# Kernel tuning notes

Measured on AMD Instinct MI355X. Metric: run time of the kernel, lower is better.

## Reference

```python
import jax, jax.numpy as jnp
import numpy as np

N_NODES = 20000
EPS_BN = 1e-5
NEG_SLOPE = 0.2


def gat_conv(x, W, att_src, att_dst, bias, src, dst, heads, out_ch, concat):
    n = x.shape[0]
    h = (x @ W).reshape(n, heads, out_ch)                       # [N,H,C]
    a_src = jnp.sum(h * att_src, axis=-1)                       # [N,H]
    a_dst = jnp.sum(h * att_dst, axis=-1)                       # [N,H]
    e = jax.nn.leaky_relu(a_src[src] + a_dst[dst], NEG_SLOPE)   # [E,H]
    # segment softmax over incoming edges of each destination node
    m = jax.ops.segment_max(e, dst, num_segments=n)             # [N,H]
    e = jnp.exp(e - m[dst])
    denom = jax.ops.segment_sum(e, dst, num_segments=n)         # [N,H]
    alpha = e / (denom[dst] + 1e-16)                            # [E,H]
    msg = alpha[:, :, None] * h[src]                            # [E,H,C]
    out = jax.ops.segment_sum(msg, dst, num_segments=n)         # [N,H,C]
    if concat:
        out = out.reshape(n, heads * out_ch)
    else:
        out = out.mean(axis=1)
    return out + bias


def batch_norm(x, gamma, beta):
    mu = x.mean(axis=0)
    var = x.var(axis=0)  # biased, matches torch normalization
    return (x - mu) * jax.lax.rsqrt(var + EPS_BN) * gamma + beta


def setup_inputs() -> dict:
    key = jax.random.key(0)
    ks = jax.random.split(key, 16)
    n, d_in, hid, heads = N_NODES, 768, 128, 8
    n_edges = 160000
    x = jax.random.normal(ks[0], (n, d_in), dtype=jnp.float32)
    edge_index = jax.random.randint(ks[1], (2, n_edges), 0, n, dtype=jnp.int64)
    s = lambda fi, fo: (2.0 / (fi + fo)) ** 0.5
    return {
        "x": x,
        "edge_index": edge_index,
        "W1": jax.random.normal(ks[2], (d_in, heads * hid), jnp.float32) * s(d_in, heads * hid),
        "att_src1": jax.random.normal(ks[3], (heads, hid), jnp.float32) * 0.1,
        "att_dst1": jax.random.normal(ks[4], (heads, hid), jnp.float32) * 0.1,
        "bias1": jnp.zeros((heads * hid,), jnp.float32),
        "bn1_g": jnp.ones((heads * hid,), jnp.float32),
        "bn1_b": jnp.zeros((heads * hid,), jnp.float32),
        "W2": jax.random.normal(ks[5], (heads * hid, hid), jnp.float32) * s(heads * hid, hid),
        "att_src2": jax.random.normal(ks[6], (1, hid), jnp.float32) * 0.1,
        "att_dst2": jax.random.normal(ks[7], (1, hid), jnp.float32) * 0.1,
        "bias2": jnp.zeros((hid,), jnp.float32),
        "bn2_g": jnp.ones((hid,), jnp.float32),
        "bn2_b": jnp.zeros((hid,), jnp.float32),
        "Wc1": jax.random.normal(ks[8], (hid, 64), jnp.float32) * s(hid, 64),
        "bc1": jnp.zeros((64,), jnp.float32),
        "Wc2": jax.random.normal(ks[9], (64, 2), jnp.float32) * s(64, 2),
        "bc2": jnp.zeros((2,), jnp.float32),
    }


def reference(x, edge_index, W1, att_src1, att_dst1, bias1, bn1_g, bn1_b,
              W2, att_src2, att_dst2, bias2, bn2_g, bn2_b,
              Wc1, bc1, Wc2, bc2):
    n = x.shape[0]
    # PyG GATConv default: add self-loops
    loops = jnp.arange(n, dtype=edge_index.dtype)
    src = jnp.concatenate([edge_index[0], loops])
    dst = jnp.concatenate([edge_index[1], loops])

    h = gat_conv(x, W1, att_src1, att_dst1, bias1, src, dst, heads=8, out_ch=128, concat=True)
    h = jax.nn.elu(batch_norm(h, bn1_g, bn1_b))
    # dropout disabled (deterministic reference)
    h = gat_conv(h, W2, att_src2, att_dst2, bias2, src, dst, heads=1, out_ch=128, concat=False)
    h = jax.nn.elu(batch_norm(h, bn2_g, bn2_b))
    h = jax.nn.elu(h @ Wc1 + bc1)
    return h @ Wc2 + bc2  # [N, 2] logits
```

## Files before the change

kernel.cpp:

```cpp
#include <hip/hip_runtime.h>
#include <stdint.h>

typedef unsigned short u16;
typedef __bf16 bf16x8 __attribute__((ext_vector_type(8)));
typedef float f32x4 __attribute__((ext_vector_type(4)));

__device__ __forceinline__ float b2f(u16 u) {
    unsigned x = ((unsigned)u) << 16;
    return __builtin_bit_cast(float, x);
}
__device__ __forceinline__ u16 f2b(float f) {
    unsigned x = __builtin_bit_cast(unsigned, f);
    x = x + 0x7fffu + ((x >> 16) & 1u);
    return (u16)(x >> 16);
}
__device__ __forceinline__ float leaky(float v) { return v > 0.f ? v : 0.2f * v; }
__device__ __forceinline__ float elu(float v) { return v > 0.f ? v : expm1f(v); }

__global__ void k_cast4(const float* __restrict__ in, u16* __restrict__ out, size_t n4) {
    size_t i = blockIdx.x * (size_t)blockDim.x + threadIdx.x;
    size_t stride = (size_t)gridDim.x * blockDim.x;
    for (; i < n4; i += stride) {
        float4 v = ((const float4*)in)[i];
        ushort4 o;
        o.x = f2b(v.x); o.y = f2b(v.y); o.z = f2b(v.z); o.w = f2b(v.w);
        ((ushort4*)out)[i] = o;
    }
}

__global__ void k_tcast(const float* __restrict__ in, u16* __restrict__ out, int R, int C) {
    __shared__ float tile[32][33];
    int tx = threadIdx.x & 31, ty = threadIdx.x >> 5;
    int c0 = blockIdx.x * 32, r0 = blockIdx.y * 32;
    #pragma unroll
    for (int i = 0; i < 32; i += 8) {
        int r = r0 + ty + i, c = c0 + tx;
        tile[ty + i][tx] = (r < R && c < C) ? in[(size_t)r * C + c] : 0.f;
    }
    __syncthreads();
    #pragma unroll
    for (int i = 0; i < 32; i += 8) {
        int c = c0 + ty + i, r = r0 + tx;
        if (c < C && r < R) out[(size_t)c * R + r] = f2b(tile[tx][ty + i]);
    }
}

#define GBM 128
#define GBN 128
#define GBK 64
#define LDT 72
#define SPLITK 4

__global__ __launch_bounds__(256) void k_gemm(const u16* __restrict__ A, const u16* __restrict__ Bt,
                                              u16* __restrict__ C, int M, int NN, int K, int nCB) {
    __shared__ __align__(16) u16 As[GBM][LDT];
    __shared__ __align__(16) u16 Bs[GBN][LDT];
    int nwg = gridDim.x, orig = blockIdx.x;
    int q = nwg >> 3, r8 = nwg & 7, xcd = orig & 7, sub = orig >> 3;
    int wgid = (xcd < r8 ? xcd * (q + 1) : r8 * (q + 1) + (xcd - r8) * q) + sub;
    int rb = wgid / nCB, cb = wgid % nCB;
    int brow = rb * GBM, bcol = cb * GBN;

    int t = threadIdx.x;
    int lane = t & 63, wid = t >> 6;
    int wm = (wid >> 1) * 64, wn = (wid & 1) * 64;
    int fr = lane & 15, fq = lane >> 4;
    f32x4 acc[4][4] = {};
    int tr = t >> 3, tc = (t & 7) * 8;
    int nK = K / GBK;
    for (int kt = 0; kt < nK; ++kt) {
        int k0 = kt * GBK;
        #pragma unroll
        for (int rr = 0; rr < 4; ++rr) {
            int r = tr + rr * 32;
            int grow = brow + r;
            uint4 bv = *reinterpret_cast<const uint4*>(Bt + (size_t)(bcol + r) * K + k0 + tc);
            *reinterpret_cast<uint4*>(&Bs[r][tc]) = bv;
            uint4 av = make_uint4(0, 0, 0, 0);
            if (grow < M) av = *reinterpret_cast<const uint4*>(A + (size_t)grow * K + k0 + tc);
            *reinterpret_cast<uint4*>(&As[r][tc]) = av;
        }
        __syncthreads();
        #pragma unroll
        for (int kk = 0; kk < 2; ++kk) {
            int ko = kk * 32 + fq * 8;
            bf16x8 af[4], bg[4];
            #pragma unroll
            for (int i = 0; i < 4; ++i) {
                af[i] = *reinterpret_cast<const bf16x8*>(&As[wm + i * 16 + fr][ko]);
                bg[i] = *reinterpret_cast<const bf16x8*>(&Bs[wn + i * 16 + fr][ko]);
            }
            #pragma unroll
            for (int mi = 0; mi < 4; ++mi)
                #pragma unroll
                for (int ni = 0; ni < 4; ++ni)
                    acc[mi][ni] = __builtin_amdgcn_mfma_f32_16x16x32_bf16(af[mi], bg[ni], acc[mi][ni], 0, 0, 0);
        }
        __syncthreads();
    }
    #pragma unroll
    for (int mi = 0; mi < 4; ++mi) {
        #pragma unroll
        for (int j = 0; j < 4; ++j) {
            int row = brow + wm + mi * 16 + fq * 4 + j;
            if (row < M) {
                #pragma unroll
                for (int ni = 0; ni < 4; ++ni) {
                    int col = bcol + wn + ni * 16 + fr;
                    C[(size_t)row * NN + col] = f2b(acc[mi][ni][j]);
                }
            }
        }
    }
}

__global__ __launch_bounds__(256) void k_gemm2(const u16* __restrict__ A, const u16* __restrict__ Bt,
                                               float* __restrict__ Cp, int M, int K,
                                               const float* __restrict__ scA, const float* __restrict__ shA) {
    __shared__ __align__(16) u16 As[GBM][LDT];
    __shared__ __align__(16) u16 Bs[GBN][LDT];
    int brow = blockIdx.x * GBM;
    int ks = blockIdx.y;
    int kBase = ks * (K / SPLITK);
    int t = threadIdx.x;
    int lane = t & 63, wid = t >> 6;
    int wm = (wid >> 1) * 64, wn = (wid & 1) * 64;
    int fr = lane & 15, fq = lane >> 4;
    f32x4 acc[4][4] = {};
    int tr = t >> 3, tc = (t & 7) * 8;
    const int nK = 1024 / SPLITK / GBK;
    for (int kt = 0; kt < nK; ++kt) {
        int k0 = kBase + kt * GBK;
        #pragma unroll
        for (int rr = 0; rr < 4; ++rr) {
            int r = tr + rr * 32;
            int grow = brow + r;
            uint4 bv = *reinterpret_cast<const uint4*>(Bt + (size_t)r * K + k0 + tc);
            *reinterpret_cast<uint4*>(&Bs[r][tc]) = bv;
            uint4 av = make_uint4(0, 0, 0, 0);
            if (grow < M) {
                uint4 u = *reinterpret_cast<const uint4*>(A + (size_t)grow * K + k0 + tc);
                float4 s0 = *(const float4*)(scA + k0 + tc);
                float4 s1 = *(const float4*)(scA + k0 + tc + 4);
                float4 h0 = *(const float4*)(shA + k0 + tc);
                float4 h1 = *(const float4*)(shA + k0 + tc + 4);
                u16 w0 = f2b(elu(b2f((u16)(u.x & 0xffff)) * s0.x + h0.x));
                u16 w1 = f2b(elu(b2f((u16)(u.x >> 16))    * s0.y + h0.y));
                u16 w2 = f2b(elu(b2f((u16)(u.y & 0xffff)) * s0.z + h0.z));
                u16 w3 = f2b(elu(b2f((u16)(u.y >> 16))    * s0.w + h0.w));
                u16 w4 = f2b(elu(b2f((u16)(u.z & 0xffff)) * s1.x + h1.x));
                u16 w5 = f2b(elu(b2f((u16)(u.z >> 16))    * s1.y + h1.y));
                u16 w6 = f2b(elu(b2f((u16)(u.w & 0xffff)) * s1.z + h1.z));
                u16 w7 = f2b(elu(b2f((u16)(u.w >> 16))    * s1.w + h1.w));
                av.x = (unsigned)w0 | ((unsigned)w1 << 16);
                av.y = (unsigned)w2 | ((unsigned)w3 << 16);
                av.z = (unsigned)w4 | ((unsigned)w5 << 16);
                av.w = (unsigned)w6 | ((unsigned)w7 << 16);
            }
            *reinterpret_cast<uint4*>(&As[r][tc]) = av;
        }
        __syncthreads();
        #pragma unroll
        for (int kk = 0; kk < 2; ++kk) {
            int ko = kk * 32 + fq * 8;
            bf16x8 af[4], bg[4];
            #pragma unroll
            for (int i = 0; i < 4; ++i) {
                af[i] = *reinterpret_cast<const bf16x8*>(&As[wm + i * 16 + fr][ko]);
                bg[i] = *reinterpret_cast<const bf16x8*>(&Bs[wn + i * 16 + fr][ko]);
            }
            #pragma unroll
            for (int mi = 0; mi < 4; ++mi)
                #pragma unroll
                for (int ni = 0; ni < 4; ++ni)
                    acc[mi][ni] = __builtin_amdgcn_mfma_f32_16x16x32_bf16(af[mi], bg[ni], acc[mi][ni], 0, 0, 0);
        }
        __syncthreads();
    }
    float* base = Cp + (size_t)ks * M * 128;
    #pragma unroll
    for (int mi = 0; mi < 4; ++mi) {
        #pragma unroll
        for (int j = 0; j < 4; ++j) {
            int row = brow + wm + mi * 16 + fq * 4 + j;
            if (row < M) {
                #pragma unroll
                for (int ni = 0; ni < 4; ++ni) {
                    int col = wn + ni * 16 + fr;
                    base[(size_t)row * 128 + col] = acc[mi][ni][j];
                }
            }
        }
    }
}

__global__ __launch_bounds__(256) void k_red2(const float* __restrict__ Cp,
                                              const float* __restrict__ attS, const float* __restrict__ attD,
                                              u16* __restrict__ h2b, float* __restrict__ asrc,
                                              float* __restrict__ adst, int M) {
    int t = threadIdx.x, lane = t & 63, wid = t >> 6;
    int row = blockIdx.x * 4 + wid;
    if (row >= M) return;
    int c = lane * 2;
    float s0 = 0.f, s1 = 0.f;
    #pragma unroll
    for (int s = 0; s < SPLITK; ++s) {
        float2 v = *(const float2*)(Cp + ((size_t)s * M + row) * 128 + c);
        s0 += v.x; s1 += v.y;
    }
    ushort2 o; o.x = f2b(s0); o.y = f2b(s1);
    *(ushort2*)(h2b + (size_t)row * 128 + c) = o;
    float ps = s0 * attS[c] + s1 * attS[c + 1];
    float pd = s0 * attD[c] + s1 * attD[c + 1];
    #pragma unroll
    for (int m = 1; m < 64; m <<= 1) { ps += __shfl_xor(ps, m); pd += __shfl_xor(pd, m); }
    if (lane == 0) { asrc[row] = ps; adst[row] = pd; }
}

__global__ void k_att8(const u16* __restrict__ h, const float* __restrict__ attS,
                       const float* __restrict__ attD, float* __restrict__ asrc,
                       float* __restrict__ adst, int N) {
    int t = threadIdx.x;
    int half = t >> 7, i = t & 127;
    int row = blockIdx.x * 2 + half;
    if (row >= N) return;
    int head = i >> 4, g = i & 15;
    const u16* hp = h + (size_t)row * 1024 + head * 128 + g * 8;
    const float* sp = attS + head * 128 + g * 8;
    const float* dp = attD + head * 128 + g * 8;
    ushort4 u0 = *(const ushort4*)hp;
    ushort4 u1 = *(const ushort4*)(hp + 4);
    float hv[8] = {b2f(u0.x), b2f(u0.y), b2f(u0.z), b2f(u0.w),
                   b2f(u1.x), b2f(u1.y), b2f(u1.z), b2f(u1.w)};
    float ps = 0.f, pd = 0.f;
    #pragma unroll
    for (int j = 0; j < 8; ++j) { ps += hv[j] * sp[j]; pd += hv[j] * dp[j]; }
    #pragma unroll
    for (int m = 1; m < 16; m <<= 1) { ps += __shfl_xor(ps, m); pd += __shfl_xor(pd, m); }
    if (g == 0) { asrc[row * 8 + head] = ps; adst[row * 8 + head] = pd; }
}

__global__ void k_detect(const int* __restrict__ ei, int* flag, int E0) {
    if (threadIdx.x == 0) *flag = 0;
    __syncthreads();
    int lim = E0 < 4096 ? E0 : 4096;
    int any = 0;
    for (int i = threadIdx.x; i < lim; i += 256) any |= (ei[2 * i + 1] != 0);
    if (any) atomicOr(flag, 1);
}

__global__ void k_deg(const int* __restrict__ ei, const int* __restrict__ flag,
                      int* __restrict__ deg, int E0, int E) {
    bool i64 = (*flag == 0);
    for (int e = blockIdx.x * blockDim.x + threadIdx.x; e < E; e += gridDim.x * blockDim.x) {
        int d;
        if (e < E0) d = i64 ? ei[2 * (E0 + e)] : ei[E0 + e];
        else d = e - E0;
        atomicAdd(&deg[d], 1);
    }
}

__global__ __launch_bounds__(1024) void k_scan(const int* __restrict__ deg, int* __restrict__ off,
                                               int* __restrict__ cursor, int n) {
    __shared__ int part[1024];
    int t = threadIdx.x;
    int chunk = (n + 1023) >> 10;
    int beg = t * chunk, end = beg + chunk;
    if (end > n) end = n;
    int s = 0;
    for (int i = beg; i < end; ++i) s += deg[i];
    part[t] = s;
    __syncthreads();
    for (int d = 1; d < 1024; d <<= 1) {
        int v = (t >= d) ? part[t - d] : 0;
        __syncthreads();
        part[t] += v;
        __syncthreads();
    }
    int run = (t == 0) ? 0 : part[t - 1];
    for (int i = beg; i < end; ++i) { off[i] = run; cursor[i] = run; run += deg[i]; }
    if (t == 1023) off[n] = part[1023];
}

__global__ void k_scatter(const int* __restrict__ ei, const int* __restrict__ flag,
                          int* __restrict__ cursor, int* __restrict__ csr, int E0, int E) {
    bool i64 = (*flag == 0);
    for (int e = blockIdx.x * blockDim.x + threadIdx.x; e < E; e += gridDim.x * blockDim.x) {
        int s, d;
        if (e < E0) {
            if (i64) { s = ei[2 * e]; d = ei[2 * (E0 + e)]; }
            else     { s = ei[e];     d = ei[E0 + e]; }
        } else { s = d = e - E0; }
        int pos = atomicAdd(&cursor[d], 1);
        csr[pos] = s;
    }
}

template <int HEADS>
__global__ __launch_bounds__(256) void k_alpha(const int* __restrict__ off, const int* __restrict__ csr,
                                               const float* __restrict__ asrc, const float* __restrict__ adst,
                                               float* __restrict__ pbuf, float* __restrict__ invb, int N) {
    const int EPC = 64 / HEADS;
    int t = threadIdx.x, lane = t & 63, wid = t >> 6;
    int node = blockIdx.x * 4 + wid;
    if (node >= N) return;
    int h = lane & (HEADS - 1);
    int e = lane / HEADS;
    float ad = adst[(size_t)node * HEADS + h];
    int lo = off[node], hi = off[node + 1];
    float m = -1e30f;
    for (int i = lo + e; i < hi; i += EPC) {
        int s = csr[i];
        float v = leaky(asrc[(size_t)s * HEADS + h] + ad);
        m = fmaxf(m, v);
    }
    #pragma unroll
    for (int mask = HEADS; mask < 64; mask <<= 1) m = fmaxf(m, __shfl_xor(m, mask));
    float ssum = 0.f;
    for (int i = lo + e; i < hi; i += EPC) {
        int s = csr[i];
        float v = leaky(asrc[(size_t)s * HEADS + h] + ad);
        float p = __expf(v - m);
        pbuf[(size_t)i * HEADS + h] = p;
        ssum += p;
    }
    #pragma unroll
    for (int mask = HEADS; mask < 64; mask <<= 1) ssum += __shfl_xor(ssum, mask);
    if (lane < HEADS) invb[(size_t)node * HEADS + h] = 1.f / (ssum + 1e-16f);
}

__global__ __launch_bounds__(256) void k_agg1(const int* __restrict__ off, const int* __restrict__ csr,
                                              const float* __restrict__ pbuf, const float* __restrict__ invb,
                                              const u16* __restrict__ h1, u16* __restrict__ outg, int N) {
    int node = blockIdx.x;
    if (node >= N) return;
    int t = threadIdx.x;
    int hh = t >> 5;
    int c0 = t * 4;
    int lo = off[node], hi = off[node + 1];
    float a0 = 0.f, a1 = 0.f, a2 = 0.f, a3 = 0.f;
    for (int i = lo; i < hi; ++i) {
        int s = csr[i];
        float p = pbuf[(size_t)i * 8 + hh];
        ushort4 u = *(const ushort4*)(h1 + (size_t)s * 1024 + c0);
        a0 += p * b2f(u.x); a1 += p * b2f(u.y);
        a2 += p * b2f(u.z); a3 += p * b2f(u.w);
    }
    float inv = invb[(size_t)node * 8 + hh];
    ushort4 o;
    o.x = f2b(a0 * inv); o.y = f2b(a1 * inv); o.z = f2b(a2 * inv); o.w = f2b(a3 * inv);
    *(ushort4*)(outg + (size_t)node * 1024 + c0) = o;
}

__global__ __launch_bounds__(256) void k_agg2(const int* __restrict__ off, const int* __restrict__ csr,
                                              const float* __restrict__ pbuf, const float* __restrict__ invb,
                                              const u16* __restrict__ h2, u16* __restrict__ outg, int N) {
    int t = threadIdx.x;
    int half = t >> 7, c = t & 127;
    int node = blockIdx.x * 2 + half;
    if (node >= N) return;
    int lo = off[node], hi = off[node + 1];
    float acc = 0.f;
    for (int i = lo; i < hi; ++i) {
        int s = csr[i];
        acc += pbuf[i] * b2f(h2[(size_t)s * 128 + c]);
    }
    outg[(size_t)node * 128 + c] = f2b(acc * invb[node]);
}

template <int CH>
__global__ __launch_bounds__(256) void k_bnpart(const u16* __restrict__ g, float* __restrict__ ps,
                                                float* __restrict__ ps2, int Nrows, int rowsPerChunk) {
    const int TPR = CH / 4;
    const int RPI = 256 / TPR;
    int t = threadIdx.x;
    int rl = t / TPR, c4 = (t % TPR) * 4;
    int chunk = blockIdx.x;
    int r0 = chunk * rowsPerChunk;
    int r1 = r0 + rowsPerChunk; if (r1 > Nrows) r1 = Nrows;
    float s[4] = {0.f, 0.f, 0.f, 0.f}, s2[4] = {0.f, 0.f, 0.f, 0.f};
    for (int r = r0 + rl; r < r1; r += RPI) {
        ushort4 u = *(const ushort4*)(g + (size_t)r * CH + c4);
        float v0 = b2f(u.x), v1 = b2f(u.y), v2 = b2f(u.z), v3 = b2f(u.w);
        s[0] += v0; s2[0] += v0 * v0;
        s[1] += v1; s2[1] += v1 * v1;
        s[2] += v2; s2[2] += v2 * v2;
        s[3] += v3; s2[3] += v3 * v3;
    }
    size_t prow = (size_t)(chunk * RPI + rl) * CH + c4;
    *(float4*)(ps + prow)  = make_float4(s[0], s[1], s[2], s[3]);
    *(float4*)(ps2 + prow) = make_float4(s2[0], s2[1], s2[2], s2[3]);
}

__global__ __launch_bounds__(256) void k_bnfinal(const float* __restrict__ ps, const float* __restrict__ ps2,
                                                 const float* __restrict__ gamma, const float* __restrict__ beta,
                                                 float* __restrict__ scale, float* __restrict__ shift,
                                                 int P, int CH, int Nrows) {
    int t = threadIdx.x, lane = t & 63, wid = t >> 6;
    int col = blockIdx.x * 4 + wid;
    if (col >= CH) return;
    float s = 0.f, s2 = 0.f;
    for (int p = lane; p < P; p += 64) {
        s += ps[(size_t)p * CH + col];
        s2 += ps2[(size_t)p * CH + col];
    }
    #pragma unroll
    for (int m = 1; m < 64; m <<= 1) { s += __shfl_xor(s, m); s2 += __shfl_xor(s2, m); }
    if (lane == 0) {
        double mu = (double)s / Nrows;
        double var = (double)s2 / Nrows - mu * mu;
        if (var < 0) var = 0;
        float sc = gamma[col] * rsqrtf((float)var + 1e-5f);
        scale[col] = sc;
        shift[col] = beta[col] - (float)mu * sc;
    }
}

__global__ __launch_bounds__(256) void k_cls(const u16* __restrict__ g2raw,
                                             const float* __restrict__ scale2, const float* __restrict__ shift2,
                                             const float* __restrict__ Wc1, const float* __restrict__ bc1,
                                             const float* __restrict__ Wc2, const float* __restrict__ bc2,
                                             float* __restrict__ out, int N) {
    __shared__ float wl[128 * 64];
    __shared__ float hs[4][128];
    int t = threadIdx.x, lane = t & 63, wid = t >> 6;
    for (int i = t; i < 128 * 64; i += 256) wl[i] = Wc1[i];
    float sc0 = scale2[2 * lane], sc1 = scale2[2 * lane + 1];
    float sh0 = shift2[2 * lane], sh1 = shift2[2 * lane + 1];
    float bb = bc1[lane];
    float c2a = Wc2[lane * 2], c2b = Wc2[lane * 2 + 1];
    float o2a = bc2[0], o2b = bc2[1];
    __syncthreads();
    int row0 = blockIdx.x * 64;
    for (int it = 0; it < 16; ++it) {
        int row = row0 + it * 4 + wid;
        if (row >= N) continue;
        const u16* hp = g2raw + (size_t)row * 128 + 2 * lane;
        float y0 = b2f(hp[0]) * sc0 + sh0; y0 = y0 > 0.f ? y0 : expm1f(y0);
        float y1 = b2f(hp[1]) * sc1 + sh1; y1 = y1 > 0.f ? y1 : expm1f(y1);
        hs[wid][2 * lane] = y0;
        hs[wid][2 * lane + 1] = y1;
        float tj = bb;
        #pragma unroll 8
        for (int c = 0; c < 128; ++c) tj += hs[wid][c] * wl[c * 64 + lane];
        tj = tj > 0.f ? tj : expm1f(tj);
        float v0 = tj * c2a, v1 = tj * c2b;
        #pragma unroll
        for (int m = 1; m < 64; m <<= 1) { v0 += __shfl_xor(v0, m); v1 += __shfl_xor(v1, m); }
        if (lane == 0) {
            out[(size_t)row * 2 + 0] = v0 + o2a;
            out[(size_t)row * 2 + 1] = v1 + o2b;
        }
    }
}

extern "C" void kernel_launch(void* const* d_in, const int* in_sizes, int n_in,
                              void* d_out, int out_size, void* d_ws, size_t ws_size,
                              hipStream_t stream) {
    const float* x     = (const float*)d_in[0];
    const int*   ei    = (const int*)d_in[1];
    const float* W1    = (const float*)d_in[2];
    const float* attS1 = (const float*)d_in[3];
    const float* attD1 = (const float*)d_in[4];
    const float* bn1g  = (const float*)d_in[6];
    const float* bn1b  = (const float*)d_in[7];
    const float* W2    = (const float*)d_in[8];
    const float* attS2 = (const float*)d_in[9];
    const float* attD2 = (const float*)d_in[10];
    const float* bn2g  = (const float*)d_in[12];
    const float* bn2b  = (const float*)d_in[13];
    const float* Wc1   = (const float*)d_in[14];
    const float* bc1   = (const float*)d_in[15];
    const float* Wc2   = (const float*)d_in[16];
    const float* bc2   = (const float*)d_in[17];
    float* out = (float*)d_out;

    const int DIN = 768, F1 = 1024, C2 = 128;
    const int N = in_sizes[0] / DIN;
    const int E0 = in_sizes[1] / 2;
    const int E = E0 + N;
    const int nMB = (N + GBM - 1) / GBM;

    char* w = (char*)d_ws;
    auto take = [&](size_t bytes) -> void* {
        void* p = (void*)w;
        w += (bytes + 255) & ~(size_t)255;
        return p;
    };
    u16* xb     = (u16*)take((size_t)N * DIN * 2);
    u16* bufA   = (u16*)take((size_t)N * F1 * 2);
    u16* h1b    = (u16*)take((size_t)N * F1 * 2);
    u16* w1t    = (u16*)take((size_t)F1 * DIN * 2);
    u16* w2t    = (u16*)take((size_t)C2 * F1 * 2);
    float* asrc1 = (float*)take((size_t)N * 8 * 4);
    float* adst1 = (float*)take((size_t)N * 8 * 4);
    int* deg    = (int*)take((size_t)N * 4);
    int* off    = (int*)take((size_t)(N + 1) * 4);
    int* cursor = (int*)take((size_t)N * 4);
    int* csr    = (int*)take((size_t)E * 4);
    int* flag   = (int*)take(256);
    u16* h2b    = (u16*)take((size_t)N * C2 * 2);
    float* asrc2 = (float*)take((size_t)N * 4);
    float* adst2 = (float*)take((size_t)N * 4);
    u16* g2     = (u16*)take((size_t)N * C2 * 2);
    float* scale1 = (float*)take(F1 * 4);
    float* shift1 = (float*)take(F1 * 4);
    float* scale2 = (float*)take(C2 * 4);
    float* shift2 = (float*)take(C2 * 4);
    float* pbuf  = (float*)take((size_t)E * 8 * 4);
    float* invb1 = (float*)take((size_t)N * 8 * 4);
    float* invb2 = (float*)take((size_t)N * 4);
    float* psA   = (float*)take((size_t)1024 * 1024 * 4);
    float* psB   = (float*)take((size_t)1024 * 1024 * 4);
    float* part  = (float*)h1b;

    hipMemsetAsync(deg, 0, (size_t)N * 4, stream);
    k_detect<<<1, 256, 0, stream>>>(ei, flag, E0);

    k_cast4<<<2048, 256, 0, stream>>>(x, xb, (size_t)N * DIN / 4);
    k_tcast<<<dim3(F1 / 32, DIN / 32), 256, 0, stream>>>(W1, w1t, DIN, F1);
    k_tcast<<<dim3(C2 / 32, F1 / 32), 256, 0, stream>>>(W2, w2t, F1, C2);

    k_gemm<<<nMB * (F1 / GBN), 256, 0, stream>>>(xb, w1t, h1b, N, F1, DIN, F1 / GBN);
    k_att8<<<(N + 1) / 2, 256, 0, stream>>>(h1b, attS1, attD1, asrc1, adst1, N);

    k_deg<<<512, 256, 0, stream>>>(ei, flag, deg, E0, E);
    k_scan<<<1, 1024, 0, stream>>>(deg, off, cursor, N);
    k_scatter<<<512, 256, 0, stream>>>(ei, flag, cursor, csr, E0, E);

    k_alpha<8><<<(N + 3) / 4, 256, 0, stream>>>(off, csr, asrc1, adst1, pbuf, invb1, N);
    k_agg1<<<N, 256, 0, stream>>>(off, csr, pbuf, invb1, h1b, bufA, N);
    {
        int nchunk = 256, rpc = (N + nchunk - 1) / nchunk;
        k_bnpart<1024><<<nchunk, 256, 0, stream>>>(bufA, psA, psB, N, rpc);
        k_bnfinal<<<F1 / 4, 256, 0, stream>>>(psA, psB, bn1g, bn1b, scale1, shift1, nchunk, F1, N);
    }

    k_gemm2<<<dim3(nMB, SPLITK), 256, 0, stream>>>(bufA, w2t, part, N, F1, scale1, shift1);
    k_red2<<<(N + 3) / 4, 256, 0, stream>>>(part, attS2, attD2, h2b, asrc2, adst2, N);

    k_alpha<1><<<(N + 3) / 4, 256, 0, stream>>>(off, csr, asrc2, adst2, pbuf, invb2, N);
    k_agg2<<<(N + 1) / 2, 256, 0, stream>>>(off, csr, pbuf, invb2, h2b, g2, N);
    {
        int nchunk = 128, rpc = (N + nchunk - 1) / nchunk;
        k_bnpart<128><<<nchunk, 256, 0, stream>>>(g2, psA, psB, N, rpc);
        k_bnfinal<<<C2 / 4, 256, 0, stream>>>(psA, psB, bn2g, bn2b, scale2, shift2, nchunk * 8, C2, N);
    }

    k_cls<<<(N + 63) / 64, 256, 0, stream>>>(g2, scale2, shift2, Wc1, bc1, Wc2, bc2, out, N);
}
```

Measured before the change: 385.3 us.

## Use direct-to-LDS swizzled loads in GEMM and fuse layer-1 softmax into aggregation

The first GEMM now stages tiles with global_load_lds 16-byte direct-to-LDS loads. It uses an XOR-swizzled, unpadded LDS layout to avoid bank conflicts, and the input buffer is padded to a multiple of the tile height so the row bounds check can go. Separately, the layer-1 edge softmax kernel is removed. The aggregation kernel now computes the max, the exponentials (in 64-edge chunks staged in shared memory) and the normalizer itself, which avoids the E×8 float pbuf round trip and one launch. The cost is extra block syncs per chunk and serialized score computation on one wave. Also, the padded xb rows are never zeroed, so their contents are undefined, though those output rows are masked.

New measurement: 366.7 us. 1.05x faster.

```diff
diff --git a/kernel.cpp b/kernel.cpp
--- a/kernel.cpp
+++ b/kernel.cpp
@@ -16,6 +16,11 @@
 }
 __device__ __forceinline__ float leaky(float v) { return v > 0.f ? v : 0.2f * v; }
 __device__ __forceinline__ float elu(float v) { return v > 0.f ? v : expm1f(v); }
+
+__device__ __forceinline__ void gload16(const u16* g, u16* l) {
+    __builtin_amdgcn_global_load_lds((const __attribute__((address_space(1))) void*)(const void*)g,
+                                     (__attribute__((address_space(3))) void*)(void*)l, 16, 0, 0);
+}
 
 __global__ void k_cast4(const float* __restrict__ in, u16* __restrict__ out, size_t n4) {
     size_t i = blockIdx.x * (size_t)blockDim.x + threadIdx.x;
@@ -53,42 +58,41 @@
 
 __global__ __launch_bounds__(256) void k_gemm(const u16* __restrict__ A, const u16* __restrict__ Bt,
                                               u16* __restrict__ C, int M, int NN, int K, int nCB) {
-    __shared__ __align__(16) u16 As[GBM][LDT];
-    __shared__ __align__(16) u16 Bs[GBN][LDT];
+    __shared__ __align__(16) u16 As[GBM][GBK];
+    __shared__ __align__(16) u16 Bs[GBN][GBK];
     int nwg = gridDim.x, orig = blockIdx.x;
     int q = nwg >> 3, r8 = nwg & 7, xcd = orig & 7, sub = orig >> 3;
     int wgid = (xcd < r8 ? xcd * (q + 1) : r8 * (q + 1) + (xcd - r8) * q) + sub;
     int rb = wgid / nCB, cb = wgid % nCB;
     int brow = rb * GBM, bcol = cb * GBN;
 
-    int t = threadIdx.x;
-    int lane = t & 63, wid = t >> 6;
+    int t = threadIdx.x, lane = t & 63, wid = t >> 6;
     int wm = (wid >> 1) * 64, wn = (wid & 1) * 64;
     int fr = lane & 15, fq = lane >> 4;
     f32x4 acc[4][4] = {};
-    int tr = t >> 3, tc = (t & 7) * 8;
+    int srow = lane >> 3;
+    int scol = (((lane & 7) ^ srow)) * 8;
+    int dcol = (lane & 7) * 8;
     int nK = K / GBK;
     for (int kt = 0; kt < nK; ++kt) {
         int k0 = kt * GBK;
         #pragma unroll
-        for (int rr = 0; rr < 4; ++rr) {
-            int r = tr + rr * 32;
-            int grow = brow + r;
-            uint4 bv = *reinterpret_cast<const uint4*>(Bt + (size_t)(bcol + r) * K + k0 + tc);
-            *reinterpret_cast<uint4*>(&Bs[r][tc]) = bv;
-            uint4 av = make_uint4(0, 0, 0, 0);
-            if (grow < M) av = *reinterpret_cast<const uint4*>(A + (size_t)grow * K + k0 + tc);
-            *reinterpret_cast<uint4*>(&As[r][tc]) = av;
+        for (int cc = 0; cc < 8; ++cc) {
+            int c = wid * 8 + cc;
+            int r = (c & 15) * 8 + srow;
+            if (c < 16) gload16(A + (size_t)(brow + r) * K + k0 + scol, &As[r][dcol]);
+            else        gload16(Bt + (size_t)(bcol + r) * K + k0 + scol, &Bs[r][dcol]);
         }
         __syncthreads();
         #pragma unroll
         for (int kk = 0; kk < 2; ++kk) {
             int ko = kk * 32 + fq * 8;
+            int kos = ko ^ ((fr & 7) << 3);
             bf16x8 af[4], bg[4];
             #pragma unroll
             for (int i = 0; i < 4; ++i) {
-                af[i] = *reinterpret_cast<const bf16x8*>(&As[wm + i * 16 + fr][ko]);
-                bg[i] = *reinterpret_cast<const bf16x8*>(&Bs[wn + i * 16 + fr][ko]);
+                af[i] = *reinterpret_cast<const bf16x8*>(&As[wm + i * 16 + fr][kos]);
+                bg[i] = *reinterpret_cast<const bf16x8*>(&Bs[wn + i * 16 + fr][kos]);
             }
             #pragma unroll
             for (int mi = 0; mi < 4; ++mi)
@@ -330,23 +334,51 @@
 }
 
 __global__ __launch_bounds__(256) void k_agg1(const int* __restrict__ off, const int* __restrict__ csr,
-                                              const float* __restrict__ pbuf, const float* __restrict__ invb,
+                                              const float* __restrict__ asrc, const float* __restrict__ adst,
                                               const u16* __restrict__ h1, u16* __restrict__ outg, int N) {
+    __shared__ float pch[64][8];
+    __shared__ float invs[8];
     int node = blockIdx.x;
     if (node >= N) return;
-    int t = threadIdx.x;
+    int t = threadIdx.x, lane = t & 63, wid = t >> 6;
     int hh = t >> 5;
     int c0 = t * 4;
     int lo = off[node], hi = off[node + 1];
+    float ad_l = 0.f, mmax = -1e30f, ssum = 0.f;
+    int h = lane & 7, es = lane >> 3;
+    if (wid == 0) {
+        ad_l = adst[(size_t)node * 8 + h];
+        for (int i = lo + es; i < hi; i += 8)
+            mmax = fmaxf(mmax, leaky(asrc[(size_t)csr[i] * 8 + h] + ad_l));
+        #pragma unroll
+        for (int mask = 8; mask < 64; mask <<= 1) mmax = fmaxf(mmax, __shfl_xor(mmax, mask));
+    }
     float a0 = 0.f, a1 = 0.f, a2 = 0.f, a3 = 0.f;
-    for (int i = lo; i < hi; ++i) {
-        int s = csr[i];
-        float p = pbuf[(size_t)i * 8 + hh];
-        ushort4 u = *(const ushort4*)(h1 + (size_t)s * 1024 + c0);
-        a0 += p * b2f(u.x); a1 += p * b2f(u.y);
-        a2 += p * b2f(u.z); a3 += p * b2f(u.w);
-    }
-    float inv = invb[(size_t)node * 8 + hh];
+    for (int base = lo; base < hi; base += 64) {
+        int cend = base + 64 < hi ? base + 64 : hi;
+        if (wid == 0) {
+            for (int i = base + es; i < cend; i += 8) {
+                float p = __expf(leaky(asrc[(size_t)csr[i] * 8 + h] + ad_l) - mmax);
+                pch[i - base][h] = p;
+                ssum += p;
+            }
+        }
+        __syncthreads();
+        for (int i = base; i < cend; ++i) {
+            float p = pch[i - base][hh];
+            ushort4 u = *(const ushort4*)(h1 + (size_t)csr[i] * 1024 + c0);
+            a0 += p * b2f(u.x); a1 += p * b2f(u.y);
+            a2 += p * b2f(u.z); a3 += p * b2f(u.w);
+        }
+        __syncthreads();
+    }
+    if (wid == 0) {
+        #pragma unroll
+        for (int mask = 8; mask < 64; mask <<= 1) ssum += __shfl_xor(ssum, mask);
+        if (lane < 8) invs[lane] = 1.f / (ssum + 1e-16f);
+    }
+    __syncthreads();
+    float inv = invs[hh];
     ushort4 o;
     o.x = f2b(a0 * inv); o.y = f2b(a1 * inv); o.z = f2b(a2 * inv); o.w = f2b(a3 * inv);
     *(ushort4*)(outg + (size_t)node * 1024 + c0) = o;
@@ -480,6 +512,7 @@
     const int E0 = in_sizes[1] / 2;
     const int E = E0 + N;
     const int nMB = (N + GBM - 1) / GBM;
+    const int Mp = nMB * GBM;
 
     char* w = (char*)d_ws;
     auto take = [&](size_t bytes) -> void* {
@@ -487,7 +520,7 @@
         w += (bytes + 255) & ~(size_t)255;
         return p;
     };
-    u16* xb     = (u16*)take((size_t)N * DIN * 2);
+    u16* xb     = (u16*)take((size_t)Mp * DIN * 2);
     u16* bufA   = (u16*)take((size_t)N * F1 * 2);
     u16* h1b    = (u16*)take((size_t)N * F1 * 2);
     u16* w1t    = (u16*)take((size_t)F1 * DIN * 2);
@@ -507,8 +540,7 @@
     float* shift1 = (float*)take(F1 * 4);
     float* scale2 = (float*)take(C2 * 4);
     float* shift2 = (float*)take(C2 * 4);
-    float* pbuf  = (float*)take((size_t)E * 8 * 4);
-    float* invb1 = (float*)take((size_t)N * 8 * 4);
+    float* pbuf  = (float*)take((size_t)E * 4);
     float* invb2 = (float*)take((size_t)N * 4);
     float* psA   = (float*)take((size_t)1024 * 1024 * 4);
     float* psB   = (float*)take((size_t)1024 * 1024 * 4);
@@ -528,8 +560,7 @@
     k_scan<<<1, 1024, 0, stream>>>(deg, off, cursor, N);
     k_scatter<<<512, 256, 0, stream>>>(ei, flag, cursor, csr, E0, E);
 
-    k_alpha<8><<<(N + 3) / 4, 256, 0, stream>>>(off, csr, asrc1, adst1, pbuf, invb1, N);
-    k_agg1<<<N, 256, 0, stream>>>(off, csr, pbuf, invb1, h1b, bufA, N);
+    k_agg1<<<N, 256, 0, stream>>>(off, csr, asrc1, adst1, h1b, bufA, N);
     {
         int nchunk = 256, rpc = (N + nchunk - 1) / nchunk;
         k_bnpart<1024><<<nchunk, 256, 0, stream>>>(bufA, psA, psB, N, rpc);
```
